# Kernel optimization log

Hardware: AMD Instinct MI355X
Metric: run time of the kernel (lower is better)

## Reference

```python
import jax, jax.numpy as jnp
import numpy as np

B, DIM, HID = 16384, 512, 256
DT, N_STEPS = 0.1, 3


def setup_inputs() -> dict:
    key = jax.random.key(0)
    ks = jax.random.split(key, 5)
    z = jax.random.normal(ks[0], (B, DIM), dtype=jnp.float32)
    # HNN energy MLP: 2*DIM -> HID -> HID -> 1 (tanh activations)
    s1 = 1.0 / np.sqrt(2 * DIM)
    s2 = 1.0 / np.sqrt(HID)
    W1 = jax.random.normal(ks[1], (2 * DIM, HID), dtype=jnp.float32) * s1
    b1 = jnp.zeros((HID,), dtype=jnp.float32)
    W2 = jax.random.normal(ks[2], (HID, HID), dtype=jnp.float32) * s2
    b2 = jnp.zeros((HID,), dtype=jnp.float32)
    W3 = jax.random.normal(ks[3], (HID, 1), dtype=jnp.float32) * s2
    b3 = jnp.zeros((1,), dtype=jnp.float32)
    return {"z": z, "W1": W1, "b1": b1, "W2": W2, "b2": b2, "W3": W3, "b3": b3}


def reference(z, W1, b1, W2, b2, W3, b3):
    d = z.shape[-1]
    dt = jnp.float32(DT)

    def H_sum(zp):  # total Hamiltonian over the batch -> scalar
        h = jnp.tanh(zp @ W1 + b1)
        h = jnp.tanh(h @ W2 + b2)
        return jnp.sum(h @ W3 + b3)

    gradH = jax.grad(H_sum)  # [B, 2d]: (dH/dq, dH/dp) per sample

    def leapfrog(zp):
        q, p = zp[:, :d], zp[:, d:]
        # half-step momentum: dp/dt = -dH/dq
        g = gradH(jnp.concatenate([q, p], axis=-1))
        p = p - 0.5 * dt * g[:, :d]
        # full-step position: dq/dt = dH/dp
        g = gradH(jnp.concatenate([q, p], axis=-1))
        q = q + dt * g[:, d:]
        # half-step momentum
        g = gradH(jnp.concatenate([q, p], axis=-1))
        p = p - 0.5 * dt * g[:, :d]
        return jnp.concatenate([q, p], axis=-1)

    zp = jnp.concatenate([z, jnp.zeros_like(z)], axis=-1)  # phase space [B, 2d]
    for _ in range(N_STEPS):  # fixed small unroll (n_steps=3)
        zp = leapfrog(zp)
    return zp[:, :d]
```

## Files before the change

kernel.cpp:

```cpp
#include <hip/hip_runtime.h>
#include <math.h>

#define DT 0.1f

typedef __attribute__((ext_vector_type(4)))  short short4v;
typedef __attribute__((ext_vector_type(8)))  short short8;
typedef __attribute__((ext_vector_type(16))) float f32x16;

__device__ __forceinline__ short f2bf(float x) {
    unsigned int u = __float_as_uint(x);
    unsigned int r = (u + 0x7fffu + ((u >> 16) & 1u)) >> 16;
    return (short)r;
}
__device__ __forceinline__ float bf2f(short s) {
    return __uint_as_float(((unsigned int)(unsigned short)s) << 16);
}
__device__ __forceinline__ float tanh_fast(float x) {
    float e = __expf(x + x);
    float r = __builtin_amdgcn_rcpf(e + 1.f);
    return __builtin_fmaf(-2.f, r, 1.f);
}

__global__ __launch_bounds__(256)
void pack32_direct(const float* __restrict__ W, short* __restrict__ out, int K, int N)
{
    int idx = blockIdx.x * 256 + threadIdx.x;
    int j = idx & 7, lane = (idx >> 3) & 63, rest = idx >> 9;
    int KT = K >> 4;
    int kt = rest % KT, nt = rest / KT;
    int k = kt * 16 + (lane >> 5) * 8 + j;
    int n = nt * 32 + (lane & 31);
    out[idx] = f2bf(W[k * N + n]);
}
__global__ __launch_bounds__(256)
void pack32_trans(const float* __restrict__ W, short* __restrict__ out, int K, int N)
{
    int idx = blockIdx.x * 256 + threadIdx.x;
    int j = idx & 7, lane = (idx >> 3) & 63, rest = idx >> 9;
    int KT = K >> 4;
    int kt = rest % KT, nt = rest / KT;
    int k = kt * 16 + (lane >> 5) * 8 + j;
    int n = nt * 32 + (lane & 31);
    out[idx] = f2bf(W[n * K + k]);
}

__global__ __launch_bounds__(256)
void pack_zA(const float* __restrict__ z, short* __restrict__ out)
{
    __shared__ short zb[32 * 520];
    const int tid = threadIdx.x;
    const int bx = blockIdx.x;
#pragma unroll
    for (int j = 0; j < 16; ++j) {
        int lin = j * 256 + tid;
        int r = lin >> 7, c4 = lin & 127;
        float4 v = ((const float4*)z)[(size_t)(bx * 32 + r) * 128 + c4];
        short4v pk;
        pk.x = f2bf(v.x); pk.y = f2bf(v.y); pk.z = f2bf(v.z); pk.w = f2bf(v.w);
        *(short4v*)&zb[r * 520 + c4 * 4] = pk;
    }
    __syncthreads();
    const int lane = tid & 63, w = tid >> 6;
    const int m = lane & 31, lh = lane >> 5;
#pragma unroll
    for (int j = 0; j < 8; ++j) {
        int kt = w * 8 + j;
        short8 f = *(const short8*)&zb[m * 520 + kt * 16 + lh * 8];
        *(short8*)(out + (((size_t)bx * 32 + kt) * 64 + lane) * 8) = f;
    }
}

__global__ __launch_bounds__(256)
void compute_S(const float* __restrict__ W1, float* __restrict__ Sq, float* __restrict__ Sp)
{
    int n = threadIdx.x;
    int b = blockIdx.x;
    float s = 0.f;
    if (b < 256) {
        int k = b;
        for (int c = 0; c < 512; ++c)
            s = __builtin_fmaf(W1[c * 256 + k], W1[(512 + c) * 256 + n], s);
        Sq[k * 256 + n] = -0.5f * DT * s;
    } else {
        int k = b - 256;
        for (int c = 0; c < 512; ++c)
            s = __builtin_fmaf(W1[(512 + c) * 256 + k], W1[c * 256 + n], s);
        Sp[k * 256 + n] = DT * s;
    }
}

__device__ __forceinline__ short8 lds_frag(const short* Ac, int kt, int mt2,
                                           int l31, int lh, int rot)
{
    int nt_s = kt >> 1;
    int po = (((kt & 1) * 2 + lh) * 4 + rot) & 15;
    int base = ((nt_s * 2 + mt2) * 64 + l31) * 16 + po;
    short4v x = *(const short4v*)&Ac[base];
    short4v y = *(const short4v*)&Ac[base + 512];
    short8 r;
    r[0] = x.x; r[1] = x.y; r[2] = x.z; r[3] = x.w;
    r[4] = y.x; r[5] = y.y; r[6] = y.z; r[7] = y.w;
    return r;
}
__device__ __forceinline__ void store_tile(short* Ac, int nt, int mt2, int lane,
                                           int rot, const f32x16 v)
{
    int base = ((nt * 2 + mt2) * 64 + lane) * 16;
#pragma unroll
    for (int c = 0; c < 4; ++c) {
        short4v pk;
        pk.x = f2bf(v[4 * c + 0]); pk.y = f2bf(v[4 * c + 1]);
        pk.z = f2bf(v[4 * c + 2]); pk.w = f2bf(v[4 * c + 3]);
        *(short4v*)&Ac[base + ((4 * c + rot) & 15)] = pk;
    }
}

__device__ __forceinline__ void gemm_nt(const short* Ac, int l31, int lh, int rot,
                                        const short8* __restrict__ Bf,
                                        f32x16& acc0, f32x16& acc1)
{
    short8 pb[4];
#pragma unroll
    for (int k = 0; k < 4; ++k) pb[k] = Bf[k * 64];
    short8 pa0 = lds_frag(Ac, 0, 0, l31, lh, rot);
    short8 pa1 = lds_frag(Ac, 0, 1, l31, lh, rot);
#pragma unroll
    for (int kt = 0; kt < 16; ++kt) {
        short8 ca0 = pa0, ca1 = pa1, cb = pb[kt & 3];
        if (kt + 4 < 16) pb[kt & 3] = Bf[(kt + 4) * 64];
        if (kt + 1 < 16) {
            pa0 = lds_frag(Ac, kt + 1, 0, l31, lh, rot);
            pa1 = lds_frag(Ac, kt + 1, 1, l31, lh, rot);
        }
        acc0 = __builtin_amdgcn_mfma_f32_32x32x16_bf16(ca0, cb, acc0, 0, 0, 0);
        acc1 = __builtin_amdgcn_mfma_f32_32x32x16_bf16(ca1, cb, acc1, 0, 0, 0);
    }
}

__global__ __launch_bounds__(512, 2)
void mega(const short* __restrict__ zpA,
          const short* __restrict__ PB1q,
          const short* __restrict__ PB2,
          const short* __restrict__ PB2T,
          const short* __restrict__ PBSq,
          const short* __restrict__ PBSp,
          const float* __restrict__ b1,
          const float* __restrict__ b2,
          const float* __restrict__ W3,
          short* __restrict__ dsumP)
{
    __shared__ short h1_c[16384];
    __shared__ short da_c[16384];

    const int tid = threadIdx.x;
    const int lane = tid & 63, w = tid >> 6;
    const int l31 = lane & 31, lh = lane >> 5;
    const int rot = ((l31 >> 2) & 3) * 4;
    const int bx = blockIdx.x;

    const int col = w * 32 + l31;
    const float b1v = b1[col], b2v = b2[col], w3v = W3[col];

    f32x16 A1[2];  A1[0] = 0.f; A1[1] = 0.f;
    f32x16 dsum[2]; dsum[0] = 0.f; dsum[1] = 0.f;

    {
        const short8* Af0 = (const short8*)zpA + ((size_t)(bx * 2 + 0) * 32) * 64 + lane;
        const short8* Af1 = (const short8*)zpA + ((size_t)(bx * 2 + 1) * 32) * 64 + lane;
        const short8* Bf  = (const short8*)PB1q + ((size_t)w * 32) * 64 + lane;
        short8 pa0[2], pa1[2], pb[4];
#pragma unroll
        for (int k = 0; k < 2; ++k) { pa0[k] = Af0[k * 64]; pa1[k] = Af1[k * 64]; }
#pragma unroll
        for (int k = 0; k < 4; ++k) pb[k] = Bf[k * 64];
#pragma unroll
        for (int kt = 0; kt < 32; ++kt) {
            short8 ca0 = pa0[kt & 1], ca1 = pa1[kt & 1], cb = pb[kt & 3];
            if (kt + 2 < 32) {
                pa0[kt & 1] = Af0[(kt + 2) * 64];
                pa1[kt & 1] = Af1[(kt + 2) * 64];
            }
            if (kt + 4 < 32) pb[kt & 3] = Bf[(kt + 4) * 64];
            A1[0] = __builtin_amdgcn_mfma_f32_32x32x16_bf16(ca0, cb, A1[0], 0, 0, 0);
            A1[1] = __builtin_amdgcn_mfma_f32_32x32x16_bf16(ca1, cb, A1[1], 0, 0, 0);
        }
    }

    for (int it = 0; it < 8; ++it) {
        const bool isq = ((it % 3) == 1);

#pragma unroll
        for (int t = 0; t < 2; ++t) {
            f32x16 hv;
#pragma unroll
            for (int r = 0; r < 16; ++r) hv[r] = tanh_fast(A1[t][r] + b1v);
            store_tile(h1_c, w, t, lane, rot, hv);
        }
        __syncthreads();

        {
            f32x16 t0 = 0.f, t1 = 0.f;
            gemm_nt(h1_c, l31, lh, rot, (const short8*)PB2 + ((size_t)w * 16) * 64 + lane, t0, t1);
#pragma unroll
            for (int t = 0; t < 2; ++t) {
                f32x16& tt = t ? t1 : t0;
                f32x16 d;
#pragma unroll
                for (int r = 0; r < 16; ++r) {
                    float ta = tanh_fast(tt[r] + b2v);
                    d[r] = w3v * (1.f - ta * ta);
                }
                store_tile(da_c, w, t, lane, rot, d);
            }
        }
        __syncthreads();

        {
            f32x16 t0 = 0.f, t1 = 0.f;
            gemm_nt(da_c, l31, lh, rot, (const short8*)PB2T + ((size_t)w * 16) * 64 + lane, t0, t1);
            __syncthreads();
#pragma unroll
            for (int t = 0; t < 2; ++t) {
                f32x16& tt = t ? t1 : t0;
                f32x16 d;
                const int basei = ((w * 2 + t) * 64 + lane) * 16;
#pragma unroll
                for (int c = 0; c < 4; ++c) {
                    short4v h4 = *(const short4v*)&h1_c[basei + ((4 * c + rot) & 15)];
                    float h0 = bf2f(h4.x), h1f = bf2f(h4.y);
                    float h2 = bf2f(h4.z), h3 = bf2f(h4.w);
                    d[4 * c + 0] = tt[4 * c + 0] * (1.f - h0 * h0);
                    d[4 * c + 1] = tt[4 * c + 1] * (1.f - h1f * h1f);
                    d[4 * c + 2] = tt[4 * c + 2] * (1.f - h2 * h2);
                    d[4 * c + 3] = tt[4 * c + 3] * (1.f - h3 * h3);
                }
                if (isq) dsum[t] += d;
                store_tile(da_c, w, t, lane, rot, d);
            }
        }
        __syncthreads();

        if (it < 7) {
            const short* S = isq ? PBSp : PBSq;
            gemm_nt(da_c, l31, lh, rot, (const short8*)S + ((size_t)w * 16) * 64 + lane,
                    A1[0], A1[1]);
        }
    }

    store_tile(da_c, w, 0, lane, rot, dsum[0]);
    store_tile(da_c, w, 1, lane, rot, dsum[1]);
    __syncthreads();
    const int mt2 = w >> 2;
#pragma unroll
    for (int kk = 0; kk < 4; ++kk) {
        int kt = (w & 3) * 4 + kk;
        short8 f = lds_frag(da_c, kt, mt2, l31, lh, rot);
        *(short8*)(dsumP + (((size_t)(bx * 2 + mt2) * 16 + kt) * 64 + lane) * 8) = f;
    }
}

__global__ __launch_bounds__(512, 2)
void out_gemm(const short* __restrict__ dsumP, const short* __restrict__ PB1Tp,
              const float* __restrict__ z, float* __restrict__ out)
{
    __shared__ float Ct[32 * 512];

    const int tid = threadIdx.x;
    const int lane = tid & 63, w = tid >> 6;
    const int mt2 = w >> 2, nq = w & 3;
    const int l31 = lane & 31, lh = lane >> 5;
    const int bx = blockIdx.x;
    const int rt32 = bx * 2 + mt2;

    f32x16 acc[4];
#pragma unroll
    for (int t = 0; t < 4; ++t) acc[t] = 0.f;

    const short8* Af = (const short8*)dsumP + (size_t)rt32 * 16 * 64 + lane;
    const short8* Bf[4];
#pragma unroll
    for (int t = 0; t < 4; ++t)
        Bf[t] = (const short8*)PB1Tp + (size_t)(nq * 4 + t) * 16 * 64 + lane;

    short8 ar[2], br[2][4];
#pragma unroll
    for (int k = 0; k < 2; ++k) {
        ar[k] = Af[k * 64];
#pragma unroll
        for (int t = 0; t < 4; ++t) br[k][t] = Bf[t][k * 64];
    }
#pragma unroll
    for (int kt = 0; kt < 16; ++kt) {
        short8 a = ar[kt & 1];
        short8 bb[4];
#pragma unroll
        for (int t = 0; t < 4; ++t) bb[t] = br[kt & 1][t];
        if (kt + 2 < 16) {
            ar[kt & 1] = Af[(kt + 2) * 64];
#pragma unroll
            for (int t = 0; t < 4; ++t) br[kt & 1][t] = Bf[t][(kt + 2) * 64];
        }
#pragma unroll
        for (int t = 0; t < 4; ++t)
            acc[t] = __builtin_amdgcn_mfma_f32_32x32x16_bf16(a, bb[t], acc[t], 0, 0, 0);
    }

#pragma unroll
    for (int p = 0; p < 2; ++p) {
        if (mt2 == p) {
#pragma unroll
            for (int t = 0; t < 4; ++t) {
                const int c = (nq * 4 + t) * 32 + l31;
#pragma unroll
                for (int r = 0; r < 16; ++r) {
                    int row = (r & 3) + 8 * (r >> 2) + 4 * lh;
                    Ct[row * 512 + c] = acc[t][r];
                }
            }
        }
        __syncthreads();
#pragma unroll
        for (int j = 0; j < 8; ++j) {
            int lin = j * 512 + tid;
            int r = lin >> 7, c4 = lin & 127;
            size_t gi = (size_t)(bx * 64 + p * 32 + r) * 128 + c4;
            float4 zv = ((const float4*)z)[gi];
            float4 cv = *(const float4*)&Ct[r * 512 + c4 * 4];
            float4 ov;
            ov.x = zv.x + DT * cv.x; ov.y = zv.y + DT * cv.y;
            ov.z = zv.z + DT * cv.z; ov.w = zv.w + DT * cv.w;
            ((float4*)out)[gi] = ov;
        }
        __syncthreads();
    }
}

extern "C" void kernel_launch(void* const* d_in, const int* in_sizes, int n_in,
                              void* d_out, int out_size, void* d_ws, size_t ws_size,
                              hipStream_t stream)
{
    const float* z  = (const float*)d_in[0];
    const float* W1 = (const float*)d_in[1];
    const float* b1 = (const float*)d_in[2];
    const float* W2 = (const float*)d_in[3];
    const float* b2 = (const float*)d_in[4];
    const float* W3 = (const float*)d_in[5];
    float* out = (float*)d_out;

    float* Sq_f  = (float*)d_ws;
    float* Sp_f  = Sq_f + 65536;
    short* PB2   = (short*)(Sp_f + 65536);
    short* PB2T  = PB2   + 65536;
    short* PBSq  = PB2T  + 65536;
    short* PBSp  = PBSq  + 65536;
    short* PB1q  = PBSp  + 65536;
    short* PB1Tp = PB1q  + 131072;
    short* zpA   = PB1Tp + 131072;
    short* dsumP = zpA   + 8388608;

    compute_S<<<512, 256, 0, stream>>>(W1, Sq_f, Sp_f);
    pack32_direct<<<256, 256, 0, stream>>>(W2, PB2, 256, 256);
    pack32_trans <<<256, 256, 0, stream>>>(W2, PB2T, 256, 256);
    pack32_direct<<<256, 256, 0, stream>>>(Sq_f, PBSq, 256, 256);
    pack32_direct<<<256, 256, 0, stream>>>(Sp_f, PBSp, 256, 256);
    pack32_direct<<<512, 256, 0, stream>>>(W1, PB1q, 512, 256);
    pack32_trans <<<512, 256, 0, stream>>>(W1 + 512 * 256, PB1Tp, 256, 512);
    pack_zA<<<512, 256, 0, stream>>>(z, zpA);

    mega<<<256, 512, 0, stream>>>(zpA, PB1q, PB2, PB2T, PBSq, PBSp,
                                  b1, b2, W3, dsumP);
    out_gemm<<<256, 512, 0, stream>>>(dsumP, PB1Tp, z, out);
}
```

Baseline: 216.7 us.

## Fuse prep kernels into one launch and merge output GEMM into mega kernel

The seven weight and input packing launches plus compute_S become one prep kernel that dispatches on block index, and compute_S now writes its bf16 packed fragments directly instead of going through an fp32 intermediate. The separate out_gemm kernel is folded into mega, which reads the dsum tile from LDS instead of round-tripping it through global memory. The LDS buffers are unified so the output staging reuses them. This removes launch overhead and a global write/read of dsumP, at the cost of a longer mega kernel and heterogeneous blocks within prep.

```diff
diff --git a/kernel.cpp b/kernel.cpp
--- a/kernel.cpp
+++ b/kernel.cpp
@@ -21,71 +21,83 @@
     return __builtin_fmaf(-2.f, r, 1.f);
 }
 
-__global__ __launch_bounds__(256)
-void pack32_direct(const float* __restrict__ W, short* __restrict__ out, int K, int N)
-{
-    int idx = blockIdx.x * 256 + threadIdx.x;
+__device__ __forceinline__ void pack32_body(const float* __restrict__ W,
+                                            short* __restrict__ out,
+                                            int K, int N, int idx, bool trans)
+{
     int j = idx & 7, lane = (idx >> 3) & 63, rest = idx >> 9;
     int KT = K >> 4;
     int kt = rest % KT, nt = rest / KT;
     int k = kt * 16 + (lane >> 5) * 8 + j;
     int n = nt * 32 + (lane & 31);
-    out[idx] = f2bf(W[k * N + n]);
-}
+    out[idx] = f2bf(trans ? W[n * K + k] : W[k * N + n]);
+}
+
 __global__ __launch_bounds__(256)
-void pack32_trans(const float* __restrict__ W, short* __restrict__ out, int K, int N)
-{
-    int idx = blockIdx.x * 256 + threadIdx.x;
-    int j = idx & 7, lane = (idx >> 3) & 63, rest = idx >> 9;
-    int KT = K >> 4;
-    int kt = rest % KT, nt = rest / KT;
-    int k = kt * 16 + (lane >> 5) * 8 + j;
-    int n = nt * 32 + (lane & 31);
-    out[idx] = f2bf(W[n * K + k]);
-}
-
-__global__ __launch_bounds__(256)
-void pack_zA(const float* __restrict__ z, short* __restrict__ out)
+void prep(const float* __restrict__ W1, const float* __restrict__ W2,
+          const float* __restrict__ z,
+          short* __restrict__ PBSq, short* __restrict__ PBSp,
+          short* __restrict__ PB2, short* __restrict__ PB2T,
+          short* __restrict__ PB1q, short* __restrict__ PB1Tp,
+          short* __restrict__ zpA)
 {
     __shared__ short zb[32 * 520];
     const int tid = threadIdx.x;
-    const int bx = blockIdx.x;
-#pragma unroll
-    for (int j = 0; j < 16; ++j) {
-        int lin = j * 256 + tid;
-        int r = lin >> 7, c4 = lin & 127;
-        float4 v = ((const float4*)z)[(size_t)(bx * 32 + r) * 128 + c4];
-        short4v pk;
-        pk.x = f2bf(v.x); pk.y = f2bf(v.y); pk.z = f2bf(v.z); pk.w = f2bf(v.w);
-        *(short4v*)&zb[r * 520 + c4 * 4] = pk;
-    }
-    __syncthreads();
-    const int lane = tid & 63, w = tid >> 6;
-    const int m = lane & 31, lh = lane >> 5;
-#pragma unroll
-    for (int j = 0; j < 8; ++j) {
-        int kt = w * 8 + j;
-        short8 f = *(const short8*)&zb[m * 520 + kt * 16 + lh * 8];
-        *(short8*)(out + (((size_t)bx * 32 + kt) * 64 + lane) * 8) = f;
-    }
-}
-
-__global__ __launch_bounds__(256)
-void compute_S(const float* __restrict__ W1, float* __restrict__ Sq, float* __restrict__ Sp)
-{
-    int n = threadIdx.x;
-    int b = blockIdx.x;
-    float s = 0.f;
-    if (b < 256) {
-        int k = b;
-        for (int c = 0; c < 512; ++c)
-            s = __builtin_fmaf(W1[c * 256 + k], W1[(512 + c) * 256 + n], s);
-        Sq[k * 256 + n] = -0.5f * DT * s;
+    const int b = blockIdx.x;
+
+    if (b < 512) {
+        const int n = tid;
+        float s0 = 0.f, s1 = 0.f, s2 = 0.f, s3 = 0.f;
+        int k; float coef; short* dst;
+        if (b < 256) {
+            k = b; coef = -0.5f * DT; dst = PBSq;
+            for (int c = 0; c < 512; c += 4) {
+                s0 = __builtin_fmaf(W1[(c + 0) * 256 + k], W1[(512 + c + 0) * 256 + n], s0);
+                s1 = __builtin_fmaf(W1[(c + 1) * 256 + k], W1[(512 + c + 1) * 256 + n], s1);
+                s2 = __builtin_fmaf(W1[(c + 2) * 256 + k], W1[(512 + c + 2) * 256 + n], s2);
+                s3 = __builtin_fmaf(W1[(c + 3) * 256 + k], W1[(512 + c + 3) * 256 + n], s3);
+            }
+        } else {
+            k = b - 256; coef = DT; dst = PBSp;
+            for (int c = 0; c < 512; c += 4) {
+                s0 = __builtin_fmaf(W1[(512 + c + 0) * 256 + k], W1[(c + 0) * 256 + n], s0);
+                s1 = __builtin_fmaf(W1[(512 + c + 1) * 256 + k], W1[(c + 1) * 256 + n], s1);
+                s2 = __builtin_fmaf(W1[(512 + c + 2) * 256 + k], W1[(c + 2) * 256 + n], s2);
+                s3 = __builtin_fmaf(W1[(512 + c + 3) * 256 + k], W1[(c + 3) * 256 + n], s3);
+            }
+        }
+        float v = coef * ((s0 + s1) + (s2 + s3));
+        int kt = k >> 4, r = k & 15;
+        int lane = (r >> 3) * 32 + (n & 31), nt = n >> 5;
+        dst[(((nt * 16 + kt) * 64 + lane) << 3) + (r & 7)] = f2bf(v);
+    } else if (b < 768) {
+        pack32_body(W2, PB2, 256, 256, (b - 512) * 256 + tid, false);
+    } else if (b < 1024) {
+        pack32_body(W2, PB2T, 256, 256, (b - 768) * 256 + tid, true);
+    } else if (b < 1536) {
+        pack32_body(W1, PB1q, 512, 256, (b - 1024) * 256 + tid, false);
+    } else if (b < 2048) {
+        pack32_body(W1 + 512 * 256, PB1Tp, 256, 512, (b - 1536) * 256 + tid, true);
     } else {
-        int k = b - 256;
-        for (int c = 0; c < 512; ++c)
-            s = __builtin_fmaf(W1[(512 + c) * 256 + k], W1[c * 256 + n], s);
-        Sp[k * 256 + n] = DT * s;
+        const int bx = b - 2048;
+#pragma unroll
+        for (int j = 0; j < 16; ++j) {
+            int lin = j * 256 + tid;
+            int r = lin >> 7, c4 = lin & 127;
+            float4 v = ((const float4*)z)[(size_t)(bx * 32 + r) * 128 + c4];
+            short4v pk;
+            pk.x = f2bf(v.x); pk.y = f2bf(v.y); pk.z = f2bf(v.z); pk.w = f2bf(v.w);
+            *(short4v*)&zb[r * 520 + c4 * 4] = pk;
+        }
+        __syncthreads();
+        const int lane = tid & 63, w = tid >> 6;
+        const int m = lane & 31, lh = lane >> 5;
+#pragma unroll
+        for (int j = 0; j < 8; ++j) {
+            int kt = w * 8 + j;
+            short8 f = *(const short8*)&zb[m * 520 + kt * 16 + lh * 8];
+            *(short8*)(zpA + (((size_t)bx * 32 + kt) * 64 + lane) * 8) = f;
+        }
     }
 }
 
@@ -147,10 +159,13 @@
           const float* __restrict__ b1,
           const float* __restrict__ b2,
           const float* __restrict__ W3,
-          short* __restrict__ dsumP)
-{
-    __shared__ short h1_c[16384];
-    __shared__ short da_c[16384];
+          const short* __restrict__ PB1Tp,
+          const float* __restrict__ z,
+          float* __restrict__ out)
+{
+    __shared__ alignas(16) short smem[32768];
+    short* h1_c = smem;
+    short* da_c = smem + 16384;
 
     const int tid = threadIdx.x;
     const int lane = tid & 63, w = tid >> 6;
@@ -250,53 +265,28 @@
     store_tile(da_c, w, 0, lane, rot, dsum[0]);
     store_tile(da_c, w, 1, lane, rot, dsum[1]);
     __syncthreads();
-    const int mt2 = w >> 2;
-#pragma unroll
-    for (int kk = 0; kk < 4; ++kk) {
-        int kt = (w & 3) * 4 + kk;
-        short8 f = lds_frag(da_c, kt, mt2, l31, lh, rot);
-        *(short8*)(dsumP + (((size_t)(bx * 2 + mt2) * 16 + kt) * 64 + lane) * 8) = f;
-    }
-}
-
-__global__ __launch_bounds__(512, 2)
-void out_gemm(const short* __restrict__ dsumP, const short* __restrict__ PB1Tp,
-              const float* __restrict__ z, float* __restrict__ out)
-{
-    __shared__ float Ct[32 * 512];
-
-    const int tid = threadIdx.x;
-    const int lane = tid & 63, w = tid >> 6;
+
     const int mt2 = w >> 2, nq = w & 3;
-    const int l31 = lane & 31, lh = lane >> 5;
-    const int bx = blockIdx.x;
-    const int rt32 = bx * 2 + mt2;
-
     f32x16 acc[4];
 #pragma unroll
     for (int t = 0; t < 4; ++t) acc[t] = 0.f;
-
-    const short8* Af = (const short8*)dsumP + (size_t)rt32 * 16 * 64 + lane;
     const short8* Bf[4];
 #pragma unroll
     for (int t = 0; t < 4; ++t)
         Bf[t] = (const short8*)PB1Tp + (size_t)(nq * 4 + t) * 16 * 64 + lane;
 
-    short8 ar[2], br[2][4];
-#pragma unroll
-    for (int k = 0; k < 2; ++k) {
-        ar[k] = Af[k * 64];
+    short8 br[2][4];
+#pragma unroll
+    for (int k = 0; k < 2; ++k)
 #pragma unroll
         for (int t = 0; t < 4; ++t) br[k][t] = Bf[t][k * 64];
-    }
 #pragma unroll
     for (int kt = 0; kt < 16; ++kt) {
-        short8 a = ar[kt & 1];
+        short8 a = lds_frag(da_c, kt, mt2, l31, lh, rot);
         short8 bb[4];
 #pragma unroll
         for (int t = 0; t < 4; ++t) bb[t] = br[kt & 1][t];
         if (kt + 2 < 16) {
-            ar[kt & 1] = Af[(kt + 2) * 64];
 #pragma unroll
             for (int t = 0; t < 4; ++t) br[kt & 1][t] = Bf[t][(kt + 2) * 64];
         }
@@ -304,7 +294,9 @@
         for (int t = 0; t < 4; ++t)
             acc[t] = __builtin_amdgcn_mfma_f32_32x32x16_bf16(a, bb[t], acc[t], 0, 0, 0);
     }
-
+    __syncthreads();
+
+    float* Ct = (float*)smem;
 #pragma unroll
     for (int p = 0; p < 2; ++p) {
         if (mt2 == p) {
@@ -347,27 +339,16 @@
     const float* W3 = (const float*)d_in[5];
     float* out = (float*)d_out;
 
-    float* Sq_f  = (float*)d_ws;
-    float* Sp_f  = Sq_f + 65536;
-    short* PB2   = (short*)(Sp_f + 65536);
+    short* PB2   = (short*)d_ws;
     short* PB2T  = PB2   + 65536;
     short* PBSq  = PB2T  + 65536;
     short* PBSp  = PBSq  + 65536;
     short* PB1q  = PBSp  + 65536;
     short* PB1Tp = PB1q  + 131072;
     short* zpA   = PB1Tp + 131072;
-    short* dsumP = zpA   + 8388608;
-
-    compute_S<<<512, 256, 0, stream>>>(W1, Sq_f, Sp_f);
-    pack32_direct<<<256, 256, 0, stream>>>(W2, PB2, 256, 256);
-    pack32_trans <<<256, 256, 0, stream>>>(W2, PB2T, 256, 256);
-    pack32_direct<<<256, 256, 0, stream>>>(Sq_f, PBSq, 256, 256);
-    pack32_direct<<<256, 256, 0, stream>>>(Sp_f, PBSp, 256, 256);
-    pack32_direct<<<512, 256, 0, stream>>>(W1, PB1q, 512, 256);
-    pack32_trans <<<512, 256, 0, stream>>>(W1 + 512 * 256, PB1Tp, 256, 512);
-    pack_zA<<<512, 256, 0, stream>>>(z, zpA);
-
+
+    prep<<<2560, 256, 0, stream>>>(W1, W2, z, PBSq, PBSp, PB2, PB2T,
+                                   PB1q, PB1Tp, zpA);
     mega<<<256, 512, 0, stream>>>(zpA, PB1q, PB2, PB2T, PBSq, PBSp,
-                                  b1, b2, W3, dsumP);
-    out_gemm<<<256, 512, 0, stream>>>(dsumP, PB1Tp, z, out);
-}
+                                  b1, b2, W3, PB1Tp, z, out);
+}
```

Result: faster. 194.2 us (-10.4%).
